# Optimization experiments

Measured on AMD Instinct MI355X. Metric: run time of the kernel, lower is better.

The kernel has to match this reference:

```python
import jax, jax.numpy as jnp
import numpy as np

B, G, K, N = 8, 2048, 32, 6
C = 64  # lc_x feature dim (mapping_size), must be even
SCALE = 10.0
EPS = 1e-8


def setup_inputs() -> dict:
    key = jax.random.key(0)
    k1, k2, k3 = jax.random.split(key, 3)
    lc_x = jax.random.normal(k1, (B, G, C), dtype=jnp.float32)
    knn_x = jax.random.normal(k2, (B, G, K, N), dtype=jnp.float32)
    fourier_B = jax.random.normal(k3, (7, C // 2), dtype=jnp.float32) * SCALE
    return {"lc_x": lc_x, "knn_x": knn_x, "fourier_B": fourier_B}


def reference(lc_x, knn_x, fourier_B):
    # lc_x: [B,G,C], knn_x: [B,G,K,N], fourier_B: [7, C//2]
    lc_normal = lc_x[:, :, 3:6][:, :, None, :]            # [B,G,1,3], broadcasts over K
    lc_line = lc_x / jnp.linalg.norm(lc_x, axis=2, keepdims=True)
    lc_line = jnp.transpose(lc_line, (0, 2, 1))            # [B,C,G]

    knn_product = knn_x[..., 3:6]                          # [B,G,K,3]
    lcn_b = jnp.broadcast_to(lc_normal, knn_product.shape)
    knn_cross = jnp.cross(knn_product, lcn_b, axis=-1)     # [B,G,K,3]
    knn_dot = jnp.sum(knn_product * lc_normal, axis=-1, keepdims=True)  # [B,G,K,1]
    knn_line = jnp.concatenate([knn_product, knn_cross, knn_dot], axis=-1)  # [B,G,K,7]

    # Fourier feature mapping (4D path: permute to channels-last already holds)
    x_proj = knn_line @ fourier_B                          # [B,G,K,C/2]
    ff = jnp.concatenate([jnp.sin(2 * jnp.pi * x_proj), jnp.cos(2 * jnp.pi * x_proj)], axis=-1)
    ff = jnp.sign(ff) * jnp.abs(ff) ** 5                   # [B,G,K,C]
    knn_f = jnp.transpose(ff, (0, 3, 1, 2))                # [B,C,G,K]

    # K_ANP over last dim (K); torch.std is unbiased (ddof=1); .item() -> stop_gradient
    std = jnp.std(knn_f, axis=-1, keepdims=True, ddof=1)
    p = 2.0 + jax.lax.stop_gradient(jnp.log1p(jnp.mean(std)))
    norm = jnp.sum(jnp.abs(knn_f) ** p, axis=-1, keepdims=True) ** (1.0 / p)  # [B,C,G,1]
    lc = norm / (norm + EPS)  # sum over size-1 last dim equals norm itself
    e_x = jnp.exp(lc)                                      # [B,C,G,1]
    up = jnp.mean(knn_f * e_x, axis=-1)                    # [B,C,G]
    down = jnp.mean(e_x, axis=-1)                          # [B,C,G]
    anp = up / down

    kl = anp + jnp.mean(knn_f, axis=-1)                    # [B,C,G] (squeeze is no-op: B,C,G>1)
    kl = kl / jnp.linalg.norm(kl, axis=-1, keepdims=True)  # normalize over G
    line_element = kl - lc_line
    return jnp.concatenate([line_element, lc_line], axis=1)  # [B,2C,G]
```

## Files before the change

### kernel.cpp

```cpp
#include <hip/hip_runtime.h>
#include <hip/hip_bf16.h>


#if __has_builtin(__builtin_amdgcn_fractf)
  #define FRACT(x) __builtin_amdgcn_fractf(x)
#else
  #define FRACT(x) ((x) - floorf(x))
#endif

__global__ __launch_bounds__(256, 8) void line_pass1(
    const float* __restrict__ lc_x,
    const float* __restrict__ knn_x,
    const float* __restrict__ fB,
    float* __restrict__ out)
{
    const int wave = threadIdx.x >> 6;
    const int lane = threadIdx.x & 63;
    const int half = lane >> 5;
    const int jj   = lane & 31;
    const int sbid = (blockIdx.x & 7) * 256 + (blockIdx.x >> 3);
    const int bg0  = sbid * 8;
    const int b    = bg0 >> 11;
    const int g0   = bg0 & 2047;

    __shared__ __align__(16) float lcbuf[4][128];
    __shared__ __align__(16) float knbuf[4][384];
    __shared__ float klbuf[128][9];

    const float fb0 = fB[0*32 + jj];
    const float fb1 = fB[1*32 + jj];
    const float fb2 = fB[2*32 + jj];
    const float fb3 = fB[3*32 + jj];
    const float fb4 = fB[4*32 + jj];
    const float fb5 = fB[5*32 + jj];
    const float fb6 = fB[6*32 + jj];

    {
        const float4* lcsrc = (const float4*)(lc_x  + (size_t)(bg0 + wave * 2) * 64);
        const float4* knsrc = (const float4*)(knn_x + (size_t)(bg0 + wave * 2) * 192);
        float4* lcb4 = (float4*)&lcbuf[wave][0];
        float4* knb4 = (float4*)&knbuf[wave][0];
        if (lane < 32) lcb4[lane]      = lcsrc[lane];
        else           knb4[lane + 32] = knsrc[lane + 32];
        knb4[lane] = knsrc[lane];
    }
    asm volatile("s_waitcnt vmcnt(0) lgkmcnt(0)" ::: "memory");

    #pragma unroll
    for (int i = 0; i < 2; ++i) {
        const int col = wave * 2 + i;
        const float* lcr = &lcbuf[wave][i * 64];
        const float* knr = &knbuf[wave][i * 192];

        const float n0 = lcr[3];
        const float n1 = lcr[4];
        const float n2 = lcr[5];

        const float myv = lcr[lane];
        float ssum = myv * myv;
        #pragma unroll
        for (int off = 32; off; off >>= 1) ssum += __shfl_xor(ssum, off, 64);
        klbuf[64 + lane][col] = myv / sqrtf(ssum);

        const float e0 = fmaf(fb6, n0, fmaf(fb5,  n1, fmaf(fb4, -n2, fb0)));
        const float e1 = fmaf(fb6, n1, fmaf(fb5, -n0, fmaf(fb3,  n2, fb1)));
        const float e2 = fmaf(fb6, n2, fmaf(fb4,  n0, fmaf(fb3, -n1, fb2)));

        float accS0 = 0.f, accS1 = 0.f, accC0 = 0.f, accC1 = 0.f;
        const float* myk = knr + half * 6;
        #pragma unroll
        for (int t = 0; t < 16; ++t) {
            const float p0 = myk[t * 12 + 3];
            const float p1 = myk[t * 12 + 4];
            const float p2 = myk[t * 12 + 5];
            const float x = fmaf(e2, p2, fmaf(e1, p1, e0 * p0));
            const float ts = FRACT(x);
            const float tc = FRACT(x + 0.25f);
            const float s  = __builtin_amdgcn_sinf(ts);
            const float cq = __builtin_amdgcn_sinf(tc);
            const float s2 = s * s,   s4 = s2 * s2;
            const float q2 = cq * cq, q4 = q2 * q2;
            if (t & 1) { accS1 = fmaf(s4, s, accS1); accC1 = fmaf(q4, cq, accC1); }
            else       { accS0 = fmaf(s4, s, accS0); accC0 = fmaf(q4, cq, accC0); }
        }
        const float aS = accS0 + accS1;
        const float aC = accC0 + accC1;
        const float totS = aS + __shfl_xor(aS, 32, 64);
        const float totC = aC + __shfl_xor(aC, 32, 64);
        klbuf[lane][col] = (half ? totC : totS) * 0.0625f;
    }

    __syncthreads();

    const int c  = threadIdx.x >> 1;
    const int j0 = (threadIdx.x & 1) * 4;
    const float4 o = make_float4(klbuf[c][j0], klbuf[c][j0+1],
                                 klbuf[c][j0+2], klbuf[c][j0+3]);
    *(float4*)(out + ((size_t)b * 128 + c) * 2048 + g0 + j0) = o;
}

__global__ __launch_bounds__(256) void line_pass2(float* __restrict__ out)
{
    const int b = blockIdx.x >> 6;
    const int c = blockIdx.x & 63;
    float4*       kl = (float4*)(out + ((size_t)b * 128 + c) * 2048);
    const float4* ll = (const float4*)(out + ((size_t)b * 128 + 64 + c) * 2048);
    const int t = threadIdx.x;

    const float4 v0 = kl[t];
    const float4 v1 = kl[t + 256];
    float ss = v0.x*v0.x + v0.y*v0.y + v0.z*v0.z + v0.w*v0.w
             + v1.x*v1.x + v1.y*v1.y + v1.z*v1.z + v1.w*v1.w;
    #pragma unroll
    for (int off = 32; off; off >>= 1) ss += __shfl_xor(ss, off, 64);

    __shared__ float wsum[4];
    if ((t & 63) == 0) wsum[t >> 6] = ss;
    __syncthreads();
    const float tot = wsum[0] + wsum[1] + wsum[2] + wsum[3];
    const float rn  = 1.0f / sqrtf(tot);

    const float4 l0 = ll[t];
    const float4 l1 = ll[t + 256];
    kl[t]       = make_float4(fmaf(v0.x, rn, -l0.x), fmaf(v0.y, rn, -l0.y),
                              fmaf(v0.z, rn, -l0.z), fmaf(v0.w, rn, -l0.w));
    kl[t + 256] = make_float4(fmaf(v1.x, rn, -l1.x), fmaf(v1.y, rn, -l1.y),
                              fmaf(v1.z, rn, -l1.z), fmaf(v1.w, rn, -l1.w));
}

extern "C" void kernel_launch(void* const* d_in, const int* in_sizes, int n_in,
                              void* d_out, int out_size, void* d_ws, size_t ws_size,
                              hipStream_t stream) {
    const float* lc_x  = (const float*)d_in[0];
    const float* knn_x = (const float*)d_in[1];
    const float* fB    = (const float*)d_in[2];
    float* out = (float*)d_out;

    line_pass1<<<2048, 256, 0, stream>>>(lc_x, knn_x, fB, out);
    line_pass2<<<512, 256, 0, stream>>>(out);
}
```

Measured before the change: 21.49 us.

## Replace LDS staging with direct loads and readlane broadcasts in pass1

Pass1 no longer stages lc_x and knn_x rows through shared memory. Each lane loads its own values directly, and scalar readlane broadcasts supply the normal vector and per-neighbour coordinates. The inner loop changes from 16 iterations computing both sin and cos per lane to 32 iterations computing one transcendental each, with cos handled by a per-half 0.25 phase shift. This also removes the cross-half shuffle. Pass2 now issues the lc_line loads before the reduction so they overlap with it. The trade-off is strided 4-byte global loads and serial readlane instructions in place of coalesced float4 staging.

```diff
diff --git a/kernel.cpp b/kernel.cpp
--- a/kernel.cpp
+++ b/kernel.cpp
@@ -8,6 +8,10 @@
   #define FRACT(x) ((x) - floorf(x))
 #endif
 
+__device__ __forceinline__ float rlanef(float v, int l) {
+    return __int_as_float(__builtin_amdgcn_readlane(__float_as_int(v), l));
+}
+
 __global__ __launch_bounds__(256, 8) void line_pass1(
     const float* __restrict__ lc_x,
     const float* __restrict__ knn_x,
@@ -16,15 +20,12 @@
 {
     const int wave = threadIdx.x >> 6;
     const int lane = threadIdx.x & 63;
-    const int half = lane >> 5;
     const int jj   = lane & 31;
     const int sbid = (blockIdx.x & 7) * 256 + (blockIdx.x >> 3);
     const int bg0  = sbid * 8;
     const int b    = bg0 >> 11;
     const int g0   = bg0 & 2047;
 
-    __shared__ __align__(16) float lcbuf[4][128];
-    __shared__ __align__(16) float knbuf[4][384];
     __shared__ float klbuf[128][9];
 
     const float fb0 = fB[0*32 + jj];
@@ -35,59 +36,51 @@
     const float fb5 = fB[5*32 + jj];
     const float fb6 = fB[6*32 + jj];
 
-    {
-        const float4* lcsrc = (const float4*)(lc_x  + (size_t)(bg0 + wave * 2) * 64);
-        const float4* knsrc = (const float4*)(knn_x + (size_t)(bg0 + wave * 2) * 192);
-        float4* lcb4 = (float4*)&lcbuf[wave][0];
-        float4* knb4 = (float4*)&knbuf[wave][0];
-        if (lane < 32) lcb4[lane]      = lcsrc[lane];
-        else           knb4[lane + 32] = knsrc[lane + 32];
-        knb4[lane] = knsrc[lane];
-    }
-    asm volatile("s_waitcnt vmcnt(0) lgkmcnt(0)" ::: "memory");
+    const float shift = (lane >= 32) ? 0.25f : 0.0f;
 
     #pragma unroll
     for (int i = 0; i < 2; ++i) {
+        const int bg  = bg0 + wave * 2 + i;
         const int col = wave * 2 + i;
-        const float* lcr = &lcbuf[wave][i * 64];
-        const float* knr = &knbuf[wave][i * 192];
 
-        const float n0 = lcr[3];
-        const float n1 = lcr[4];
-        const float n2 = lcr[5];
+        const float myv = lc_x[(size_t)bg * 64 + lane];
+        const float n0 = rlanef(myv, 3);
+        const float n1 = rlanef(myv, 4);
+        const float n2 = rlanef(myv, 5);
 
-        const float myv = lcr[lane];
         float ssum = myv * myv;
         #pragma unroll
         for (int off = 32; off; off >>= 1) ssum += __shfl_xor(ssum, off, 64);
         klbuf[64 + lane][col] = myv / sqrtf(ssum);
 
+        const float* kp = knn_x + (size_t)bg * 192 + jj * 6;
+        const float p0 = kp[3];
+        const float p1 = kp[4];
+        const float p2 = kp[5];
+
         const float e0 = fmaf(fb6, n0, fmaf(fb5,  n1, fmaf(fb4, -n2, fb0)));
         const float e1 = fmaf(fb6, n1, fmaf(fb5, -n0, fmaf(fb3,  n2, fb1)));
         const float e2 = fmaf(fb6, n2, fmaf(fb4,  n0, fmaf(fb3, -n1, fb2)));
 
-        float accS0 = 0.f, accS1 = 0.f, accC0 = 0.f, accC1 = 0.f;
-        const float* myk = knr + half * 6;
+        float a0 = 0.f, a1 = 0.f, a2 = 0.f, a3 = 0.f;
         #pragma unroll
-        for (int t = 0; t < 16; ++t) {
-            const float p0 = myk[t * 12 + 3];
-            const float p1 = myk[t * 12 + 4];
-            const float p2 = myk[t * 12 + 5];
-            const float x = fmaf(e2, p2, fmaf(e1, p1, e0 * p0));
-            const float ts = FRACT(x);
-            const float tc = FRACT(x + 0.25f);
-            const float s  = __builtin_amdgcn_sinf(ts);
-            const float cq = __builtin_amdgcn_sinf(tc);
-            const float s2 = s * s,   s4 = s2 * s2;
-            const float q2 = cq * cq, q4 = q2 * q2;
-            if (t & 1) { accS1 = fmaf(s4, s, accS1); accC1 = fmaf(q4, cq, accC1); }
-            else       { accS0 = fmaf(s4, s, accS0); accC0 = fmaf(q4, cq, accC0); }
+        for (int t = 0; t < 32; ++t) {
+            const float sp0 = rlanef(p0, t);
+            const float sp1 = rlanef(p1, t);
+            const float sp2 = rlanef(p2, t);
+            const float x  = fmaf(e2, sp2, fmaf(e1, sp1, e0 * sp0));
+            const float tt = FRACT(x + shift);
+            const float s  = __builtin_amdgcn_sinf(tt);
+            const float s2 = s * s, s4 = s2 * s2;
+            const float v  = s4 * s;
+            switch (t & 3) {
+                case 0: a0 += v; break;
+                case 1: a1 += v; break;
+                case 2: a2 += v; break;
+                default: a3 += v; break;
+            }
         }
-        const float aS = accS0 + accS1;
-        const float aC = accC0 + accC1;
-        const float totS = aS + __shfl_xor(aS, 32, 64);
-        const float totC = aC + __shfl_xor(aC, 32, 64);
-        klbuf[lane][col] = (half ? totC : totS) * 0.0625f;
+        klbuf[lane][col] = ((a0 + a1) + (a2 + a3)) * 0.0625f;
     }
 
     __syncthreads();
@@ -109,6 +102,9 @@
 
     const float4 v0 = kl[t];
     const float4 v1 = kl[t + 256];
+    const float4 l0 = ll[t];
+    const float4 l1 = ll[t + 256];
+
     float ss = v0.x*v0.x + v0.y*v0.y + v0.z*v0.z + v0.w*v0.w
              + v1.x*v1.x + v1.y*v1.y + v1.z*v1.z + v1.w*v1.w;
     #pragma unroll
@@ -120,8 +116,6 @@
     const float tot = wsum[0] + wsum[1] + wsum[2] + wsum[3];
     const float rn  = 1.0f / sqrtf(tot);
 
-    const float4 l0 = ll[t];
-    const float4 l1 = ll[t + 256];
     kl[t]       = make_float4(fmaf(v0.x, rn, -l0.x), fmaf(v0.y, rn, -l0.y),
                               fmaf(v0.z, rn, -l0.z), fmaf(v0.w, rn, -l0.w));
     kl[t + 256] = make_float4(fmaf(v1.x, rn, -l1.x), fmaf(v1.y, rn, -l1.y),
```

Result: slower. 26.78 us (+24.6%).

## Load only needed knn components into padded LDS and use hardware cos/rsq

Applied to the files above, without the earlier changes.

Each lane now loads only the three used components (3:6) of one knn row straight from global memory and stores them as a padded float4 in LDS. This replaces the bulk copy of all six components and makes each inner-loop read a single vector LDS load. The cosine now comes from the hardware cos instruction instead of a second fract plus sin, and divide-by-sqrt is replaced by rsq in both kernels. Pass2 also issues its lc_line loads before the reduction barrier so their latency overlaps it. The risks are uncoalesced strided global reads of 12 bytes per lane and slightly lower precision from rsq and cos.

```diff
diff --git a/kernel.cpp b/kernel.cpp
--- a/kernel.cpp
+++ b/kernel.cpp
@@ -23,8 +23,8 @@
     const int b    = bg0 >> 11;
     const int g0   = bg0 & 2047;
 
-    __shared__ __align__(16) float lcbuf[4][128];
-    __shared__ __align__(16) float knbuf[4][384];
+    __shared__ __align__(16) float  lcbuf[4][128];
+    __shared__ __align__(16) float4 pbuf[4][2][32];
     __shared__ float klbuf[128][9];
 
     const float fb0 = fB[0*32 + jj];
@@ -36,21 +36,22 @@
     const float fb6 = fB[6*32 + jj];
 
     {
-        const float4* lcsrc = (const float4*)(lc_x  + (size_t)(bg0 + wave * 2) * 64);
-        const float4* knsrc = (const float4*)(knn_x + (size_t)(bg0 + wave * 2) * 192);
-        float4* lcb4 = (float4*)&lcbuf[wave][0];
-        float4* knb4 = (float4*)&knbuf[wave][0];
-        if (lane < 32) lcb4[lane]      = lcsrc[lane];
-        else           knb4[lane + 32] = knsrc[lane + 32];
-        knb4[lane] = knsrc[lane];
+        const float* kp = knn_x + (size_t)(bg0 + wave * 2 + half) * 192 + jj * 6;
+        const float gp0 = kp[3];
+        const float gp1 = kp[4];
+        const float gp2 = kp[5];
+        float4 lcv;
+        if (lane < 32)
+            lcv = ((const float4*)(lc_x + (size_t)(bg0 + wave * 2) * 64))[lane];
+        pbuf[wave][half][jj] = make_float4(gp0, gp1, gp2, 0.0f);
+        if (lane < 32) ((float4*)&lcbuf[wave][0])[lane] = lcv;
     }
-    asm volatile("s_waitcnt vmcnt(0) lgkmcnt(0)" ::: "memory");
+    asm volatile("s_waitcnt lgkmcnt(0)" ::: "memory");
 
     #pragma unroll
     for (int i = 0; i < 2; ++i) {
         const int col = wave * 2 + i;
         const float* lcr = &lcbuf[wave][i * 64];
-        const float* knr = &knbuf[wave][i * 192];
 
         const float n0 = lcr[3];
         const float n1 = lcr[4];
@@ -60,24 +61,21 @@
         float ssum = myv * myv;
         #pragma unroll
         for (int off = 32; off; off >>= 1) ssum += __shfl_xor(ssum, off, 64);
-        klbuf[64 + lane][col] = myv / sqrtf(ssum);
+        klbuf[64 + lane][col] = myv * __builtin_amdgcn_rsqf(ssum);
 
         const float e0 = fmaf(fb6, n0, fmaf(fb5,  n1, fmaf(fb4, -n2, fb0)));
         const float e1 = fmaf(fb6, n1, fmaf(fb5, -n0, fmaf(fb3,  n2, fb1)));
         const float e2 = fmaf(fb6, n2, fmaf(fb4,  n0, fmaf(fb3, -n1, fb2)));
 
         float accS0 = 0.f, accS1 = 0.f, accC0 = 0.f, accC1 = 0.f;
-        const float* myk = knr + half * 6;
+        const float4* myk = &pbuf[wave][i][half];
         #pragma unroll
         for (int t = 0; t < 16; ++t) {
-            const float p0 = myk[t * 12 + 3];
-            const float p1 = myk[t * 12 + 4];
-            const float p2 = myk[t * 12 + 5];
-            const float x = fmaf(e2, p2, fmaf(e1, p1, e0 * p0));
+            const float4 p = myk[2 * t];
+            const float x  = fmaf(e2, p.z, fmaf(e1, p.y, e0 * p.x));
             const float ts = FRACT(x);
-            const float tc = FRACT(x + 0.25f);
             const float s  = __builtin_amdgcn_sinf(ts);
-            const float cq = __builtin_amdgcn_sinf(tc);
+            const float cq = __builtin_amdgcn_cosf(ts);
             const float s2 = s * s,   s4 = s2 * s2;
             const float q2 = cq * cq, q4 = q2 * q2;
             if (t & 1) { accS1 = fmaf(s4, s, accS1); accC1 = fmaf(q4, cq, accC1); }
@@ -109,6 +107,9 @@
 
     const float4 v0 = kl[t];
     const float4 v1 = kl[t + 256];
+    const float4 l0 = ll[t];
+    const float4 l1 = ll[t + 256];
+
     float ss = v0.x*v0.x + v0.y*v0.y + v0.z*v0.z + v0.w*v0.w
              + v1.x*v1.x + v1.y*v1.y + v1.z*v1.z + v1.w*v1.w;
     #pragma unroll
@@ -118,10 +119,8 @@
     if ((t & 63) == 0) wsum[t >> 6] = ss;
     __syncthreads();
     const float tot = wsum[0] + wsum[1] + wsum[2] + wsum[3];
-    const float rn  = 1.0f / sqrtf(tot);
+    const float rn  = __builtin_amdgcn_rsqf(tot);
 
-    const float4 l0 = ll[t];
-    const float4 l1 = ll[t + 256];
     kl[t]       = make_float4(fmaf(v0.x, rn, -l0.x), fmaf(v0.y, rn, -l0.y),
                               fmaf(v0.z, rn, -l0.z), fmaf(v0.w, rn, -l0.w));
     kl[t + 256] = make_float4(fmaf(v1.x, rn, -l1.x), fmaf(v1.y, rn, -l1.y),
```

Result: faster. 19.91 us (-7.3%).
